# Optimization experiments

Measured on AMD Instinct MI355X. Metric: run time of the kernel, lower is better.

Reference implementation:

```python
import jax, jax.numpy as jnp
import numpy as np
from jax import lax

RADIUS = 8
EPS = 0.01


def box_filter(x, r):
    # Sum over a (2r+1)x(2r+1) window with zero ('same') padding — identical math
    # to depthwise conv2d with a ones kernel and padding=r.
    k = 2 * r + 1
    return lax.reduce_window(
        x, jnp.array(0, x.dtype), lax.add,
        window_dimensions=(1, 1, k, k),
        window_strides=(1, 1, 1, 1),
        padding=((0, 0), (0, 0), (r, r), (r, r)),
    )


def setup_inputs() -> dict:
    key = jax.random.key(0)
    k1, k2 = jax.random.split(key)
    shape = (16, 3, 512, 512)
    I = jax.random.uniform(k1, shape, dtype=jnp.float32)
    p = jax.random.uniform(k2, shape, dtype=jnp.float32)
    return {"I": I, "p": p}


def reference(I, p):
    r = RADIUS
    eps = EPS
    N = box_filter(jnp.ones_like(I), r)          # window pixel counts (handles borders)
    mean_I = box_filter(I, r) / N
    mean_p = box_filter(p, r) / N
    mean_Ip = box_filter(I * p, r) / N
    cov_Ip = mean_Ip - mean_I * mean_p
    mean_II = box_filter(I * I, r) / N
    var_I = mean_II - mean_I * mean_I
    a = cov_Ip / (var_I + eps)
    b = mean_p - a * mean_I
    mean_a = box_filter(a, r) / N
    mean_b = box_filter(b, r) / N
    q = mean_a * I + mean_b
    return q
```

## Files before the change

kernel.cpp:

```cpp
#include <hip/hip_runtime.h>


#define RAD  8
#define H    512
#define W    512
#define TILE 32
#define KCH  4
#define EPS  0.01f

__global__ __launch_bounds__(512, 4)
void guided_filter_kernel(const float* __restrict__ Ig,
                          const float* __restrict__ Pg,
                          float* __restrict__ out)
{
    __shared__ __align__(16) float4 F4[64 * 32];
    __shared__ __align__(16) float4 H4[64 * 48];

    float2* F2p = (float2*)F4;
    float2* AB  = (float2*)F4;
    float2* HAB = (float2*)F4 + 48 * 50;

    const int tid   = threadIdx.x;
    const int plane = blockIdx.z;
    const int x0 = blockIdx.x * TILE - 2 * RAD;
    const int Y0 = blockIdx.y * (TILE * KCH);
    const float* Ib = Ig + (size_t)plane * (H * W);
    const float* Pb = Pg + (size_t)plane * (H * W);
    float* Ob = out + (size_t)plane * (H * W);

    auto stage_raw = [&](int ybase, int nrows) {
        const int iters = (nrows * 16) >> 9;
        const bool interior = (x0 >= 0) && (x0 + 64 <= W) &&
                              (ybase >= 0) && (ybase + nrows <= H);
        if (interior) {
            for (int it = 0; it < iters; ++it) {
                int idx = it * 512 + tid;
                int ry = idx >> 4, f4 = idx & 15;
                int rl = ry & 7, pf = ry & 1;
                const float* ip = Ib + (ybase + ry) * W + x0 + 4 * f4;
                const float* pp = Pb + (ybase + ry) * W + x0 + 4 * f4;
                float4 iv = *(const float4*)ip;
                float4 pv = *(const float4*)pp;
                float2 e0 = make_float2(iv.x, pv.x), e1 = make_float2(iv.y, pv.y);
                float2 e2 = make_float2(iv.z, pv.z), e3 = make_float2(iv.w, pv.w);
                float2 a0 = pf ? e1 : e0, a1 = pf ? e0 : e1;
                float2 b0 = pf ? e3 : e2, b1 = pf ? e2 : e3;
                float4* Fr = &F4[ry * 32];
                Fr[(2 * f4) ^ rl]     = make_float4(a0.x, a0.y, a1.x, a1.y);
                Fr[(2 * f4 + 1) ^ rl] = make_float4(b0.x, b0.y, b1.x, b1.y);
            }
        } else {
            for (int it = 0; it < iters; ++it) {
                int idx = it * 512 + tid;
                int ry = idx >> 4, f4 = idx & 15;
                int rl = ry & 7, pf = ry & 1;
                int gy = ybase + ry;
                float2 el[4];
                #pragma unroll
                for (int k = 0; k < 4; ++k) {
                    int gx = x0 + 4 * f4 + k;
                    bool v = ((unsigned)gy < (unsigned)H) && ((unsigned)gx < (unsigned)W);
                    el[k].x = v ? Ib[gy * W + gx] : 0.f;
                    el[k].y = v ? Pb[gy * W + gx] : 0.f;
                }
                float2 a0 = pf ? el[1] : el[0], a1 = pf ? el[0] : el[1];
                float2 b0 = pf ? el[3] : el[2], b1 = pf ? el[2] : el[3];
                float4* Fr = &F4[ry * 32];
                Fr[(2 * f4) ^ rl]     = make_float4(a0.x, a0.y, a1.x, a1.y);
                Fr[(2 * f4 + 1) ^ rl] = make_float4(b0.x, b0.y, b1.x, b1.y);
            }
        }
    };

    auto s2_rows = [&](int tbase, bool full) {
        if (full || tid < 256) {
            const int r  = tid >> 3, e = tid & 7;
            const int rl = r & 7, pf = r & 1;
            const int c0 = 6 * e;
            const float4* Fr = &F4[r * 32];
            const float2* Er = (const float2*)Fr;
            float4 S = make_float4(0.f, 0.f, 0.f, 0.f);
            const int gb = 3 * e;
            #pragma unroll
            for (int m = 0; m < 8; ++m) {
                float4 fr = Fr[(gb + m) ^ rl];
                S.x += fr.x + fr.z;
                S.y += fr.y + fr.w;
                S.z += fr.x * fr.y + fr.z * fr.w;
                S.w += fr.x * fr.x + fr.z * fr.z;
            }
            {
                int c = c0 + 16;
                float2 v = Er[(((c >> 1) ^ rl) << 1) | pf];
                S.x += v.x; S.y += v.y; S.z += v.x * v.y; S.w += v.x * v.x;
            }
            const int slot = (tbase + r) & 63;
            float4* Hrow = &H4[slot * 48];
            #pragma unroll
            for (int k = 0; k < 6; ++k) {
                Hrow[(c0 + k) ^ rl] = S;
                if (k < 5) {
                    int ca = c0 + k + 17, cs = c0 + k;
                    float2 va = Er[(((ca >> 1) ^ rl) << 1) | ((ca & 1) ^ pf)];
                    float2 vs = Er[(((cs >> 1) ^ rl) << 1) | ((cs & 1) ^ pf)];
                    S.x += va.x - vs.x;
                    S.y += va.y - vs.y;
                    S.z += va.x * va.y - vs.x * vs.y;
                    S.w += va.x * va.x - vs.x * vs.x;
                }
            }
        }
    };

    auto s3g = [&](int g) {
        if (tid < 384) {
            const int col = tid % 48, chunk = tid / 48;
            const int cy0 = chunk * 6;
            const int tb = 32 * g;
            float4 S = make_float4(0.f, 0.f, 0.f, 0.f);
            #pragma unroll
            for (int j = 0; j < 17; ++j) {
                int row = tb + cy0 + j;
                float4 v = H4[(row & 63) * 48 + (col ^ (row & 7))];
                S.x += v.x; S.y += v.y; S.z += v.z; S.w += v.w;
            }
            int gx = x0 + RAD + col;
            int nx = min(gx + RAD, W - 1) - max(gx - RAD, 0) + 1;
            #pragma unroll
            for (int k = 0; k < 6; ++k) {
                int cy = cy0 + k;
                int gy = Y0 + 32 * g - RAD + cy;
                float a = 0.f, b = 0.f;
                if (((unsigned)gy < (unsigned)H) && ((unsigned)gx < (unsigned)W)) {
                    int ny = min(gy + RAD, H - 1) - max(gy - RAD, 0) + 1;
                    float invN = __builtin_amdgcn_rcpf((float)(nx * ny));
                    float mI = S.x * invN, mp = S.y * invN;
                    float cov = S.z * invN - mI * mp;
                    float var = S.w * invN - mI * mI;
                    a = cov * __builtin_amdgcn_rcpf(var + EPS);
                    b = mp - a * mI;
                }
                AB[cy * 50 + col] = make_float2(a, b);
                if (k < 5) {
                    int ra = tb + cy + 17, rs = tb + cy;
                    float4 va = H4[(ra & 63) * 48 + (col ^ (ra & 7))];
                    float4 vs = H4[(rs & 63) * 48 + (col ^ (rs & 7))];
                    S.x += va.x - vs.x; S.y += va.y - vs.y;
                    S.z += va.z - vs.z; S.w += va.w - vs.w;
                }
            }
        }
    };

    auto s4 = [&]() {
        if (tid < 384) {
            const int r = tid % 48, e = tid / 48;
            const int c0 = 4 * e;
            const float2* row  = &AB[r * 50];
            const float4* rowg = (const float4*)row;
            float2 S = make_float2(0.f, 0.f);
            #pragma unroll
            for (int m = 0; m < 8; ++m) {
                float4 gq = rowg[2 * e + m];
                S.x += gq.x + gq.z;
                S.y += gq.y + gq.w;
            }
            {
                float2 v = row[c0 + 16];
                S.x += v.x; S.y += v.y;
            }
            #pragma unroll
            for (int k = 0; k < 4; ++k) {
                HAB[r * 33 + c0 + k] = S;
                if (k < 3) {
                    float2 va = row[c0 + k + 17];
                    float2 vs = row[c0 + k];
                    S.x += va.x - vs.x; S.y += va.y - vs.y;
                }
            }
        }
    };

    auto s5g = [&](int g) {
        const int col = tid & 31, chunk = tid >> 5;
        const int oy0 = chunk * 2;
        float2 S = make_float2(0.f, 0.f);
        #pragma unroll
        for (int j = 0; j < 17; ++j) {
            float2 v = HAB[(oy0 + j) * 33 + col];
            S.x += v.x; S.y += v.y;
        }
        int gx = x0 + 2 * RAD + col;
        int nx = min(gx + RAD, W - 1) - max(gx - RAD, 0) + 1;
        #pragma unroll
        for (int k = 0; k < 2; ++k) {
            int oy = oy0 + k;
            int gy = Y0 + 32 * g + oy;
            int ny = min(gy + RAD, H - 1) - max(gy - RAD, 0) + 1;
            float invN = __builtin_amdgcn_rcpf((float)(nx * ny));
            float iv = Ib[gy * W + gx];
            Ob[gy * W + gx] = S.x * invN * iv + S.y * invN;
            if (k < 1) {
                float2 va = HAB[(oy + 17) * 33 + col];
                float2 vs = HAB[oy * 33 + col];
                S.x += va.x - vs.x; S.y += va.y - vs.y;
            }
        }
    };

    stage_raw(Y0 - 2 * RAD, 64);
    __syncthreads();
    s2_rows(0, true);
    #pragma unroll 1
    for (int g = 0; g < KCH; ++g) {
        __syncthreads();
        s3g(g);
        __syncthreads();
        s4();
        __syncthreads();
        if (g < KCH - 1)
            stage_raw(Y0 + 32 * g + 48, 32);
        s5g(g);
        if (g < KCH - 1) {
            __syncthreads();
            s2_rows(32 * g + 64, false);
        }
    }
}

extern "C" void kernel_launch(void* const* d_in, const int* in_sizes, int n_in,
                              void* d_out, int out_size, void* d_ws, size_t ws_size,
                              hipStream_t stream) {
    const float* I = (const float*)d_in[0];
    const float* P = (const float*)d_in[1];
    float* out = (float*)d_out;
    int planes = in_sizes[0] / (H * W);
    dim3 grid(W / TILE, H / (TILE * KCH), planes);
    guided_filter_kernel<<<grid, dim3(512), 0, stream>>>(I, P, out);
}
```

Measured before the change: 242.4 us.

## Double rows per block, precompute swizzled LDS offsets, and unroll ring-buffer parity

Raises the number of 32-row chunks each block processes from 4 to 8, which halves the grid and amortizes the halo rows recomputed at each block's top. The vertical-sum stage now precomputes swizzled byte offsets into the 64-row ring buffer and unrolls the loop by chunk parity, so the row-modulo and XOR arithmetic disappears from the inner loop. It also runs that stage with fewer threads, each covering more rows, and the output stage with 256 threads covering four rows each. The cost is fewer blocks and lower occupancy and parallelism across the GPU, plus more serial work per thread.

```diff
diff --git a/kernel.cpp b/kernel.cpp
--- a/kernel.cpp
+++ b/kernel.cpp
@@ -5,7 +5,7 @@
 #define H    512
 #define W    512
 #define TILE 32
-#define KCH  4
+#define KCH  8
 #define EPS  0.01f
 
 __global__ __launch_bounds__(512, 4)
@@ -16,7 +16,6 @@
     __shared__ __align__(16) float4 F4[64 * 32];
     __shared__ __align__(16) float4 H4[64 * 48];
 
-    float2* F2p = (float2*)F4;
     float2* AB  = (float2*)F4;
     float2* HAB = (float2*)F4 + 48 * 50;
 
@@ -112,23 +111,33 @@
         }
     };
 
-    auto s3g = [&](int g) {
-        if (tid < 384) {
-            const int col = tid % 48, chunk = tid / 48;
-            const int cy0 = chunk * 6;
-            const int tb = 32 * g;
+    auto s3g = [&](int g, int ODD) {
+        if (tid < 288) {
+            const int col = tid % 48;
+            const int cy0 = (tid / 48) * 8;
+            unsigned ab[8], ap[8], am[8];
+            #pragma unroll
+            for (int k = 0; k < 8; ++k) {
+                ab[k] = (unsigned)(cy0 * 768 + ((col ^ k) << 4));
+                ap[k] = ab[k] + 24576u;
+                am[k] = ab[k] - 24576u;
+            }
+            const char* Hb = (const char*)H4;
+            const int t = 32 - cy0;
             float4 S = make_float4(0.f, 0.f, 0.f, 0.f);
             #pragma unroll
             for (int j = 0; j < 17; ++j) {
-                int row = tb + cy0 + j;
-                float4 v = H4[(row & 63) * 48 + (col ^ (row & 7))];
+                unsigned off;
+                if (ODD) off = (j >= t ? am[j & 7] : ap[j & 7]) + (unsigned)(j * 768);
+                else     off = ab[j & 7] + (unsigned)(j * 768);
+                float4 v = *(const float4*)(Hb + off);
                 S.x += v.x; S.y += v.y; S.z += v.z; S.w += v.w;
             }
             int gx = x0 + RAD + col;
             int nx = min(gx + RAD, W - 1) - max(gx - RAD, 0) + 1;
             #pragma unroll
-            for (int k = 0; k < 6; ++k) {
-                int cy = cy0 + k;
+            for (int kk = 0; kk < 8; ++kk) {
+                const int cy = cy0 + kk;
                 int gy = Y0 + 32 * g - RAD + cy;
                 float a = 0.f, b = 0.f;
                 if (((unsigned)gy < (unsigned)H) && ((unsigned)gx < (unsigned)W)) {
@@ -141,10 +150,19 @@
                     b = mp - a * mI;
                 }
                 AB[cy * 50 + col] = make_float2(a, b);
-                if (k < 5) {
-                    int ra = tb + cy + 17, rs = tb + cy;
-                    float4 va = H4[(ra & 63) * 48 + (col ^ (ra & 7))];
-                    float4 vs = H4[(rs & 63) * 48 + (col ^ (rs & 7))];
+                if (kk < 7) {
+                    unsigned offs, offa;
+                    if (ODD) {
+                        offs = (kk >= t ? am[kk & 7] : ap[kk & 7])
+                               + (unsigned)(kk * 768);
+                        offa = (kk + 17 >= t ? am[(kk + 1) & 7] : ap[(kk + 1) & 7])
+                               + (unsigned)((kk + 17) * 768);
+                    } else {
+                        offs = ab[kk & 7] + (unsigned)(kk * 768);
+                        offa = ab[(kk + 1) & 7] + (unsigned)((kk + 17) * 768);
+                    }
+                    float4 va = *(const float4*)(Hb + offa);
+                    float4 vs = *(const float4*)(Hb + offs);
                     S.x += va.x - vs.x; S.y += va.y - vs.y;
                     S.z += va.z - vs.z; S.w += va.w - vs.w;
                 }
@@ -182,28 +200,30 @@
     };
 
     auto s5g = [&](int g) {
-        const int col = tid & 31, chunk = tid >> 5;
-        const int oy0 = chunk * 2;
-        float2 S = make_float2(0.f, 0.f);
-        #pragma unroll
-        for (int j = 0; j < 17; ++j) {
-            float2 v = HAB[(oy0 + j) * 33 + col];
-            S.x += v.x; S.y += v.y;
-        }
-        int gx = x0 + 2 * RAD + col;
-        int nx = min(gx + RAD, W - 1) - max(gx - RAD, 0) + 1;
-        #pragma unroll
-        for (int k = 0; k < 2; ++k) {
-            int oy = oy0 + k;
-            int gy = Y0 + 32 * g + oy;
-            int ny = min(gy + RAD, H - 1) - max(gy - RAD, 0) + 1;
-            float invN = __builtin_amdgcn_rcpf((float)(nx * ny));
-            float iv = Ib[gy * W + gx];
-            Ob[gy * W + gx] = S.x * invN * iv + S.y * invN;
-            if (k < 1) {
-                float2 va = HAB[(oy + 17) * 33 + col];
-                float2 vs = HAB[oy * 33 + col];
-                S.x += va.x - vs.x; S.y += va.y - vs.y;
+        if (tid < 256) {
+            const int col = tid & 31, chunk = tid >> 5;
+            const int oy0 = chunk * 4;
+            float2 S = make_float2(0.f, 0.f);
+            #pragma unroll
+            for (int j = 0; j < 17; ++j) {
+                float2 v = HAB[(oy0 + j) * 33 + col];
+                S.x += v.x; S.y += v.y;
+            }
+            int gx = x0 + 2 * RAD + col;
+            int nx = min(gx + RAD, W - 1) - max(gx - RAD, 0) + 1;
+            #pragma unroll
+            for (int k = 0; k < 4; ++k) {
+                int oy = oy0 + k;
+                int gy = Y0 + 32 * g + oy;
+                int ny = min(gy + RAD, H - 1) - max(gy - RAD, 0) + 1;
+                float invN = __builtin_amdgcn_rcpf((float)(nx * ny));
+                float iv = Ib[gy * W + gx];
+                Ob[gy * W + gx] = S.x * invN * iv + S.y * invN;
+                if (k < 3) {
+                    float2 va = HAB[(oy + 17) * 33 + col];
+                    float2 vs = HAB[oy * 33 + col];
+                    S.x += va.x - vs.x; S.y += va.y - vs.y;
+                }
             }
         }
     };
@@ -212,18 +232,33 @@
     __syncthreads();
     s2_rows(0, true);
     #pragma unroll 1
-    for (int g = 0; g < KCH; ++g) {
-        __syncthreads();
-        s3g(g);
-        __syncthreads();
-        s4();
-        __syncthreads();
-        if (g < KCH - 1)
+    for (int gp = 0; gp < KCH; gp += 2) {
+        {
+            const int g = gp;
+            __syncthreads();
+            s3g(g, 0);
+            __syncthreads();
+            s4();
+            __syncthreads();
             stage_raw(Y0 + 32 * g + 48, 32);
-        s5g(g);
-        if (g < KCH - 1) {
+            s5g(g);
             __syncthreads();
             s2_rows(32 * g + 64, false);
+        }
+        {
+            const int g = gp + 1;
+            __syncthreads();
+            s3g(g, 1);
+            __syncthreads();
+            s4();
+            __syncthreads();
+            if (g < KCH - 1)
+                stage_raw(Y0 + 32 * g + 48, 32);
+            s5g(g);
+            if (g < KCH - 1) {
+                __syncthreads();
+                s2_rows(32 * g + 64, false);
+            }
         }
     }
 }
```

New measurement: 343.1 us. 41.5% more time.
